# Performance work log

Measured on AMD Instinct MI355X. Metric: run time of the kernel, lower is better.

Reference implementation:

```python
import jax, jax.numpy as jnp
import numpy as np

GROUPS = 8


def setup_inputs() -> dict:
    key = jax.random.key(0)
    k1, k2, k3 = jax.random.split(key, 3)
    B, H, W, Cin, Cout, KH, KW = 32, 56, 56, 256, 256, 3, 3
    inputs = jax.random.normal(k1, (B, H, W, Cin), dtype=jnp.float32)
    # HWIO kernel for grouped conv: input channel dim = Cin // groups
    fan_in = KH * KW * (Cin // GROUPS)
    limit = np.sqrt(6.0 / (fan_in + Cout // GROUPS))  # glorot-ish scale
    kernel = jax.random.uniform(k2, (KH, KW, Cin // GROUPS, Cout), dtype=jnp.float32,
                                minval=-limit, maxval=limit)
    bias = jnp.zeros((Cout,), dtype=jnp.float32)
    return {"inputs": inputs, "kernel": kernel, "bias": bias}


def reference(inputs, kernel, bias):
    # Equivalent to per-group slice + Conv2D + concat: a single grouped conv.
    # inputs: [B,H,W,Cin] NHWC; kernel: [KH,KW,Cin//G,Cout] HWIO
    out = jax.lax.conv_general_dilated(
        inputs, kernel,
        window_strides=(1, 1),
        padding="SAME",
        lhs_dilation=(1, 1),
        rhs_dilation=(1, 1),
        dimension_numbers=("NHWC", "HWIO", "NHWC"),
        feature_group_count=GROUPS,
    )
    out = out + bias  # broadcast over [B,H,W,Cout]
    return out
```

## Files before the change

### kernel.cpp

```cpp
#include <hip/hip_runtime.h>


#define R_ 8
#define TPW 7

typedef __bf16 bf16x8 __attribute__((ext_vector_type(8)));
typedef float floatx4 __attribute__((ext_vector_type(4)));
typedef unsigned short ushortx4 __attribute__((ext_vector_type(4)));

__device__ __forceinline__ unsigned short f2bf(float f) {
    unsigned int u = __builtin_bit_cast(unsigned int, f);
    u += 0x7fffu + ((u >> 16) & 1u);
    return (unsigned short)(u >> 16);
}

__global__ __launch_bounds__(256)
void wprep(const float* __restrict__ wgt, unsigned short* __restrict__ wbf) {
    const int i = blockIdx.x * 256 + threadIdx.x;
    const int co256 = i & 255;
    const int tmp   = i >> 8;
    const int ci    = tmp & 31;
    const int kk    = tmp >> 5;
    const int g  = co256 >> 5;
    const int co = co256 & 31;
    wbf[((g * 9 + kk) * 32 + co) * 32 + ci] = f2bf(wgt[i]);
}

__global__ __launch_bounds__(256, 4)
void gconv_mfma(const float* __restrict__ in, const unsigned short* __restrict__ wbf,
                const float* __restrict__ bias, float* __restrict__ out) {
    const int rt = blockIdx.x;
    const int g  = blockIdx.y;
    const int b  = blockIdx.z;
    const int y0 = rt * R_;

    __shared__ unsigned short lds_in[10 * 58 * 32];

    const int tid = threadIdx.x;

    for (int c = tid; c < 10 * 58 * 8; c += 256) {
        const int row = c / 464;
        const int rem = c - row * 464;
        const int col = rem >> 3;
        const int q   = rem & 7;
        const int gy = y0 - 1 + row;
        const int gx = col - 1;
        float4 v = make_float4(0.f, 0.f, 0.f, 0.f);
        if ((unsigned)gy < 56u && (unsigned)gx < 56u) {
            v = *reinterpret_cast<const float4*>(
                &in[(((b * 56 + gy) * 56 + gx) * 256) + g * 32 + q * 4]);
        }
        ushortx4 p;
        p.x = f2bf(v.x); p.y = f2bf(v.y); p.z = f2bf(v.z); p.w = f2bf(v.w);
        *reinterpret_cast<ushortx4*>(&lds_in[(row * 58 + col) * 32 + q * 4]) = p;
    }

    __syncthreads();

    const int wv   = tid >> 6;
    const int lane = tid & 63;
    const int lc   = lane & 15;
    const int quad = lane >> 4;

    int lane_base[TPW];
#pragma unroll
    for (int t = 0; t < TPW; ++t) {
        const int p  = (wv * TPW + t) * 16 + lc;
        const int yl = p / 56;
        const int xl = p - yl * 56;
        lane_base[t] = (yl * 58 + xl) * 32 + quad * 8;
    }

    const unsigned short* wq = &wbf[((g * 9) * 32) * 32 + quad * 8];

    floatx4 acc[TPW][2];
#pragma unroll
    for (int t = 0; t < TPW; ++t) {
        acc[t][0] = (floatx4)(0.f);
        acc[t][1] = (floatx4)(0.f);
    }

    bf16x8 b0 = *reinterpret_cast<const bf16x8*>(&wq[(0 * 32 + lc) * 32]);
    bf16x8 b1 = *reinterpret_cast<const bf16x8*>(&wq[(0 * 32 + 16 + lc) * 32]);

#pragma unroll
    for (int kk = 0; kk < 9; ++kk) {
        const int ky = kk / 3, kx = kk % 3;
        const int koff = (ky * 58 + kx) * 32;
        bf16x8 nb0 = b0, nb1 = b1;
        if (kk < 8) {
            nb0 = *reinterpret_cast<const bf16x8*>(&wq[((kk + 1) * 32 + lc) * 32]);
            nb1 = *reinterpret_cast<const bf16x8*>(&wq[((kk + 1) * 32 + 16 + lc) * 32]);
        }
#pragma unroll
        for (int t = 0; t < TPW; ++t) {
            const bf16x8 a = *reinterpret_cast<const bf16x8*>(&lds_in[lane_base[t] + koff]);
            acc[t][0] = __builtin_amdgcn_mfma_f32_16x16x32_bf16(a, b0, acc[t][0], 0, 0, 0);
            acc[t][1] = __builtin_amdgcn_mfma_f32_16x16x32_bf16(a, b1, acc[t][1], 0, 0, 0);
        }
        b0 = nb0; b1 = nb1;
    }

    const float bv0 = bias[g * 32 + lc];
    const float bv1 = bias[g * 32 + 16 + lc];
#pragma unroll
    for (int t = 0; t < TPW; ++t) {
#pragma unroll
        for (int r = 0; r < 4; ++r) {
            const int p = (wv * TPW + t) * 16 + quad * 4 + r;
            const int y = p / 56;
            const int x = p - y * 56;
            float* o = &out[(((b * 56) + y0 + y) * 56 + x) * 256 + g * 32];
            o[lc]      = acc[t][0][r] + bv0;
            o[16 + lc] = acc[t][1][r] + bv1;
        }
    }
}

__global__ __launch_bounds__(256, 2)
void gconv_mfma_ldsw(const float* __restrict__ in, const float* __restrict__ wgt,
                     const float* __restrict__ bias, float* __restrict__ out) {
    const int rt = blockIdx.x, g = blockIdx.y, b = blockIdx.z;
    const int y0 = rt * R_;
    __shared__ unsigned short lds_in[10 * 58 * 32];
    __shared__ unsigned short lds_w[9 * 32 * 32];
    const int tid = threadIdx.x;
    for (int i = tid; i < 9 * 32 * 32; i += 256) {
        const int co = i & 31, ci = (i >> 5) & 31, kk = i >> 10;
        lds_w[(kk * 32 + co) * 32 + ci] = f2bf(wgt[(kk * 32 + ci) * 256 + g * 32 + co]);
    }
    for (int c = tid; c < 10 * 58 * 8; c += 256) {
        const int row = c / 464, rem = c - row * 464, col = rem >> 3, q = rem & 7;
        const int gy = y0 - 1 + row, gx = col - 1;
        float4 v = make_float4(0.f, 0.f, 0.f, 0.f);
        if ((unsigned)gy < 56u && (unsigned)gx < 56u)
            v = *reinterpret_cast<const float4*>(&in[(((b * 56 + gy) * 56 + gx) * 256) + g * 32 + q * 4]);
        ushortx4 p;
        p.x = f2bf(v.x); p.y = f2bf(v.y); p.z = f2bf(v.z); p.w = f2bf(v.w);
        *reinterpret_cast<ushortx4*>(&lds_in[(row * 58 + col) * 32 + q * 4]) = p;
    }
    __syncthreads();
    const int wv = tid >> 6, lane = tid & 63, lc = lane & 15, quad = lane >> 4;
    int lane_base[TPW];
#pragma unroll
    for (int t = 0; t < TPW; ++t) {
        const int p = (wv * TPW + t) * 16 + lc;
        const int yl = p / 56, xl = p - yl * 56;
        lane_base[t] = (yl * 58 + xl) * 32 + quad * 8;
    }
    floatx4 acc[TPW][2];
#pragma unroll
    for (int t = 0; t < TPW; ++t) { acc[t][0] = (floatx4)(0.f); acc[t][1] = (floatx4)(0.f); }
#pragma unroll
    for (int kk = 0; kk < 9; ++kk) {
        const int ky = kk / 3, kx = kk % 3;
        const int koff = (ky * 58 + kx) * 32;
        const bf16x8 bf0 = *reinterpret_cast<const bf16x8*>(&lds_w[(kk * 32 + lc) * 32 + quad * 8]);
        const bf16x8 bf1 = *reinterpret_cast<const bf16x8*>(&lds_w[(kk * 32 + 16 + lc) * 32 + quad * 8]);
#pragma unroll
        for (int t = 0; t < TPW; ++t) {
            const bf16x8 a = *reinterpret_cast<const bf16x8*>(&lds_in[lane_base[t] + koff]);
            acc[t][0] = __builtin_amdgcn_mfma_f32_16x16x32_bf16(a, bf0, acc[t][0], 0, 0, 0);
            acc[t][1] = __builtin_amdgcn_mfma_f32_16x16x32_bf16(a, bf1, acc[t][1], 0, 0, 0);
        }
    }
    const float bv0 = bias[g * 32 + lc], bv1 = bias[g * 32 + 16 + lc];
#pragma unroll
    for (int t = 0; t < TPW; ++t)
#pragma unroll
        for (int r = 0; r < 4; ++r) {
            const int p = (wv * TPW + t) * 16 + quad * 4 + r;
            const int y = p / 56, x = p - y * 56;
            float* o = &out[(((b * 56) + y0 + y) * 56 + x) * 256 + g * 32];
            o[lc] = acc[t][0][r] + bv0;
            o[16 + lc] = acc[t][1][r] + bv1;
        }
}

extern "C" void kernel_launch(void* const* d_in, const int* in_sizes, int n_in,
                              void* d_out, int out_size, void* d_ws, size_t ws_size,
                              hipStream_t stream) {
    const float* in   = (const float*)d_in[0];
    const float* wgt  = (const float*)d_in[1];
    const float* bias = (const float*)d_in[2];
    float* out        = (float*)d_out;
    dim3 grid(7, 8, 32);

    if (ws_size >= (size_t)(8 * 9 * 32 * 32 * sizeof(unsigned short))) {
        unsigned short* wbf = (unsigned short*)d_ws;
        wprep<<<dim3(288, 1, 1), dim3(256, 1, 1), 0, stream>>>(wgt, wbf);
        gconv_mfma<<<grid, dim3(256, 1, 1), 0, stream>>>(in, wbf, bias, out);
    } else {
        gconv_mfma_ldsw<<<grid, dim3(256, 1, 1), 0, stream>>>(in, wgt, bias, out);
    }
}
```

Baseline: 197.6 us.

## Batch input loads into registers, stage output through LDS for coalesced stores, swap grid order

The input halo load now issues all global loads up front into registers (8 floats per thread), then converts to bf16 and writes 16-byte LDS stores, which raises memory-level parallelism. The epilogue transposes each MFMA accumulator tile through per-wave LDS scratch so each lane writes 32 contiguous bytes per pixel instead of scattered 4-byte stores. The grid is reordered so the group index varies fastest, making adjacent blocks read adjacent channel slices. The cost is higher register pressure from the 20 float4 buffers, plus an extra barrier and LDS round trips in the epilogue.

```diff
diff --git a/kernel.cpp b/kernel.cpp
--- a/kernel.cpp
+++ b/kernel.cpp
@@ -1,12 +1,11 @@
 #include <hip/hip_runtime.h>
 
 
-#define R_ 8
 #define TPW 7
 
 typedef __bf16 bf16x8 __attribute__((ext_vector_type(8)));
 typedef float floatx4 __attribute__((ext_vector_type(4)));
-typedef unsigned short ushortx4 __attribute__((ext_vector_type(4)));
+typedef unsigned short ushortx8 __attribute__((ext_vector_type(8)));
 
 __device__ __forceinline__ unsigned short f2bf(float f) {
     unsigned int u = __builtin_bit_cast(unsigned int, f);
@@ -29,30 +28,46 @@
 __global__ __launch_bounds__(256, 4)
 void gconv_mfma(const float* __restrict__ in, const unsigned short* __restrict__ wbf,
                 const float* __restrict__ bias, float* __restrict__ out) {
-    const int rt = blockIdx.x;
-    const int g  = blockIdx.y;
+    const int g  = blockIdx.x;
+    const int rt = blockIdx.y;
     const int b  = blockIdx.z;
-    const int y0 = rt * R_;
+    const int y0 = rt * 8;
 
     __shared__ unsigned short lds_in[10 * 58 * 32];
 
     const int tid = threadIdx.x;
 
-    for (int c = tid; c < 10 * 58 * 8; c += 256) {
-        const int row = c / 464;
-        const int rem = c - row * 464;
-        const int col = rem >> 3;
-        const int q   = rem & 7;
+    float4 lo[10], hi[10];
+    int ldsoff[10];
+#pragma unroll
+    for (int i = 0; i < 10; ++i) {
+        const int gidx = tid + i * 256;
+        const bool valid = gidx < 2320;
+        const int sub = gidx & 3;
+        const int cr  = gidx >> 2;
+        const int col = cr % 58;
+        const int row = cr / 58;
         const int gy = y0 - 1 + row;
         const int gx = col - 1;
-        float4 v = make_float4(0.f, 0.f, 0.f, 0.f);
-        if ((unsigned)gy < 56u && (unsigned)gx < 56u) {
-            v = *reinterpret_cast<const float4*>(
-                &in[(((b * 56 + gy) * 56 + gx) * 256) + g * 32 + q * 4]);
-        }
-        ushortx4 p;
-        p.x = f2bf(v.x); p.y = f2bf(v.y); p.z = f2bf(v.z); p.w = f2bf(v.w);
-        *reinterpret_cast<ushortx4*>(&lds_in[(row * 58 + col) * 32 + q * 4]) = p;
+        ldsoff[i] = valid ? (row * 58 + col) * 32 + sub * 8 : -1;
+        lo[i] = make_float4(0.f, 0.f, 0.f, 0.f);
+        hi[i] = make_float4(0.f, 0.f, 0.f, 0.f);
+        if (valid && (unsigned)gy < 56u && (unsigned)gx < 56u) {
+            const float* p = &in[(((b * 56 + gy) * 56 + gx) * 256) + g * 32 + sub * 8];
+            lo[i] = *reinterpret_cast<const float4*>(p);
+            hi[i] = *reinterpret_cast<const float4*>(p + 4);
+        }
+    }
+#pragma unroll
+    for (int i = 0; i < 10; ++i) {
+        if (ldsoff[i] >= 0) {
+            ushortx8 pk;
+            pk[0] = f2bf(lo[i].x); pk[1] = f2bf(lo[i].y);
+            pk[2] = f2bf(lo[i].z); pk[3] = f2bf(lo[i].w);
+            pk[4] = f2bf(hi[i].x); pk[5] = f2bf(hi[i].y);
+            pk[6] = f2bf(hi[i].z); pk[7] = f2bf(hi[i].w);
+            *reinterpret_cast<ushortx8*>(&lds_in[ldsoff[i]]) = pk;
+        }
     }
 
     __syncthreads();
@@ -101,27 +116,38 @@
         b0 = nb0; b1 = nb1;
     }
 
+    __syncthreads();
+    float* scr = reinterpret_cast<float*>(lds_in) + wv * 576;
     const float bv0 = bias[g * 32 + lc];
     const float bv1 = bias[g * 32 + 16 + lc];
+    const int px_s = lane >> 2;
+    const int c8   = (lane & 3) * 8;
 #pragma unroll
     for (int t = 0; t < TPW; ++t) {
 #pragma unroll
         for (int r = 0; r < 4; ++r) {
-            const int p = (wv * TPW + t) * 16 + quad * 4 + r;
-            const int y = p / 56;
-            const int x = p - y * 56;
-            float* o = &out[(((b * 56) + y0 + y) * 56 + x) * 256 + g * 32];
-            o[lc]      = acc[t][0][r] + bv0;
-            o[16 + lc] = acc[t][1][r] + bv1;
-        }
+            const int px = quad * 4 + r;
+            scr[px * 36 + lc]      = acc[t][0][r] + bv0;
+            scr[px * 36 + 16 + lc] = acc[t][1][r] + bv1;
+        }
+        asm volatile("s_waitcnt lgkmcnt(0)" ::: "memory");
+        const floatx4 oa = *reinterpret_cast<const floatx4*>(&scr[px_s * 36 + c8]);
+        const floatx4 ob = *reinterpret_cast<const floatx4*>(&scr[px_s * 36 + c8 + 4]);
+        const int p = (wv * TPW + t) * 16 + px_s;
+        const int y = p / 56;
+        const int x = p - y * 56;
+        float* o = &out[(((b * 56) + y0 + y) * 56 + x) * 256 + g * 32 + c8];
+        *reinterpret_cast<floatx4*>(o)     = oa;
+        *reinterpret_cast<floatx4*>(o + 4) = ob;
+        asm volatile("s_waitcnt lgkmcnt(0)" ::: "memory");
     }
 }
 
 __global__ __launch_bounds__(256, 2)
 void gconv_mfma_ldsw(const float* __restrict__ in, const float* __restrict__ wgt,
                      const float* __restrict__ bias, float* __restrict__ out) {
-    const int rt = blockIdx.x, g = blockIdx.y, b = blockIdx.z;
-    const int y0 = rt * R_;
+    const int rt = blockIdx.y, g = blockIdx.x, b = blockIdx.z;
+    const int y0 = rt * 8;
     __shared__ unsigned short lds_in[10 * 58 * 32];
     __shared__ unsigned short lds_w[9 * 32 * 32];
     const int tid = threadIdx.x;
@@ -135,9 +161,9 @@
         float4 v = make_float4(0.f, 0.f, 0.f, 0.f);
         if ((unsigned)gy < 56u && (unsigned)gx < 56u)
             v = *reinterpret_cast<const float4*>(&in[(((b * 56 + gy) * 56 + gx) * 256) + g * 32 + q * 4]);
-        ushortx4 p;
-        p.x = f2bf(v.x); p.y = f2bf(v.y); p.z = f2bf(v.z); p.w = f2bf(v.w);
-        *reinterpret_cast<ushortx4*>(&lds_in[(row * 58 + col) * 32 + q * 4]) = p;
+        unsigned short p0 = f2bf(v.x), p1 = f2bf(v.y), p2 = f2bf(v.z), p3 = f2bf(v.w);
+        unsigned short* d = &lds_in[(row * 58 + col) * 32 + q * 4];
+        d[0] = p0; d[1] = p1; d[2] = p2; d[3] = p3;
     }
     __syncthreads();
     const int wv = tid >> 6, lane = tid & 63, lc = lane & 15, quad = lane >> 4;
@@ -184,7 +210,7 @@
     const float* wgt  = (const float*)d_in[1];
     const float* bias = (const float*)d_in[2];
     float* out        = (float*)d_out;
-    dim3 grid(7, 8, 32);
+    dim3 grid(8, 7, 32);
 
     if (ws_size >= (size_t)(8 * 9 * 32 * 32 * sizeof(unsigned short))) {
         unsigned short* wbf = (unsigned short*)d_ws;
```

After: 202.5 us. +2.5%, slower.
